# Kernel optimization log

Hardware: AMD Instinct MI355X
Metric: run time of the kernel (lower is better)

Reference implementation:

```python
import jax, jax.numpy as jnp
import numpy as np

# Static multi-scale spatial shapes (H, W) for a 640x640 input, strides [4,8,16,32]
SHAPES = [(160, 160), (80, 80), (40, 40), (20, 20)]
NUM_HEADS, NUM_LEVELS, NUM_POINTS, EMBED_DIM = 8, 4, 4, 256
HEAD_DIM = EMBED_DIM // NUM_HEADS
LEN_V = sum(h * w for h, w in SHAPES)  # 34000


def setup_inputs() -> dict:
    key = jax.random.key(0)
    ks = jax.random.split(key, 12)
    bs, lq = 8, 300
    inp = {
        "query": jax.random.normal(ks[0], (bs, lq, EMBED_DIM), jnp.float32),
        "reference_points": jax.random.uniform(ks[1], (bs, lq, NUM_LEVELS, 2), jnp.float32),
        "value": jax.random.normal(ks[2], (bs, LEN_V, EMBED_DIM), jnp.float32),
        "Wv": jax.random.normal(ks[3], (EMBED_DIM, EMBED_DIM), jnp.float32) * 0.02,
        "bv": jnp.zeros((EMBED_DIM,), jnp.float32),
        "Woff": jax.random.normal(ks[4], (NUM_HEADS * NUM_LEVELS * NUM_POINTS * 2, EMBED_DIM), jnp.float32) * 0.01,
        "boff": jax.random.normal(ks[5], (NUM_HEADS * NUM_LEVELS * NUM_POINTS * 2,), jnp.float32),
        "Wattn": jax.random.normal(ks[6], (NUM_HEADS * NUM_LEVELS * NUM_POINTS, EMBED_DIM), jnp.float32) * 0.02,
        "battn": jnp.zeros((NUM_HEADS * NUM_LEVELS * NUM_POINTS,), jnp.float32),
        "Wout": jax.random.normal(ks[7], (EMBED_DIM, EMBED_DIM), jnp.float32) * 0.02,
        "bout": jnp.zeros((EMBED_DIM,), jnp.float32),
    }
    return inp


def _bilinear_sample(v, loc, H, W):
    """grid_sample(align_corners=False, zero padding) equivalent.
    v:   [bs, H*W, nh, hd] level feature
    loc: [bs, Lq, nh, P, 2] sampling locations in [0, 1]
    returns [bs, Lq, nh, P, hd]
    """
    x = loc[..., 0] * W - 0.5
    y = loc[..., 1] * H - 0.5
    x0 = jnp.floor(x)
    y0 = jnp.floor(y)
    wx = (x - x0)[..., None]
    wy = (y - y0)[..., None]
    x0i = x0.astype(jnp.int32)
    y0i = y0.astype(jnp.int32)

    bs, _, nh, _ = v.shape
    bi = jnp.arange(bs)[:, None, None, None]
    hi = jnp.arange(nh)[None, None, :, None]

    def gather(xi, yi):
        valid = (xi >= 0) & (xi < W) & (yi >= 0) & (yi < H)
        idx = jnp.clip(yi, 0, H - 1) * W + jnp.clip(xi, 0, W - 1)  # [bs,Lq,nh,P]
        g = v[bi, idx, hi]  # [bs,Lq,nh,P,hd]
        return g * valid[..., None].astype(v.dtype)

    g00 = gather(x0i, y0i)
    g01 = gather(x0i + 1, y0i)
    g10 = gather(x0i, y0i + 1)
    g11 = gather(x0i + 1, y0i + 1)
    return (g00 * (1 - wx) * (1 - wy) + g01 * wx * (1 - wy)
            + g10 * (1 - wx) * wy + g11 * wx * wy)


def reference(query, reference_points, value, Wv, bv, Woff, boff, Wattn, battn, Wout, bout):
    bs, lq, _ = query.shape
    nh, nl, npts, hd = NUM_HEADS, NUM_LEVELS, NUM_POINTS, HEAD_DIM

    # value projection -> per-head value
    v = (value @ Wv.T + bv).reshape(bs, -1, nh, hd)

    # sampling offsets and attention weights from the query
    off = (query @ Woff.T + boff).reshape(bs, lq, nh, nl, npts, 2)
    aw = (query @ Wattn.T + battn).reshape(bs, lq, nh, nl * npts)
    aw = jax.nn.softmax(aw, axis=-1).reshape(bs, lq, nh, nl, npts)

    # normalize offsets by (W, H) per level; ref points are 2-d
    normalizer = jnp.array([[w, h] for h, w in SHAPES], jnp.float32)  # [nl,2]
    loc = reference_points[:, :, None, :, None, :] + off / normalizer[None, None, None, :, None, :]

    out = jnp.zeros((bs, lq, nh, hd), query.dtype)
    start = 0
    for l, (H, W) in enumerate(SHAPES):
        v_l = jax.lax.dynamic_slice_in_dim(v, start, H * W, axis=1)
        sampled = _bilinear_sample(v_l, loc[:, :, :, l], H, W)  # [bs,Lq,nh,P,hd]
        out = out + jnp.einsum("bqhp,bqhpd->bqhd", aw[:, :, :, l], sampled)
        start += H * W

    out = out.reshape(bs, lq, nh * hd)
    return out @ Wout.T + bout
```

## Files before the change

kernel.cpp:

```cpp
#include <hip/hip_runtime.h>
#include <hip/hip_bf16.h>


#define BS 8
#define LQ 300
#define LEN_V 34000
#define ED 256
#define NH 8
#define NL 4
#define NP 4

#define VSTRIPS 2125

typedef short short8 __attribute__((ext_vector_type(8)));
typedef short sv4 __attribute__((ext_vector_type(4)));
typedef float f32x4 __attribute__((ext_vector_type(4)));

__device__ __forceinline__ short8 cvt8_reg(float4 a, float4 b) {
  union { short8 v; __hip_bfloat16 h[8]; } u;
  u.h[0] = __float2bfloat16(a.x); u.h[1] = __float2bfloat16(a.y);
  u.h[2] = __float2bfloat16(a.z); u.h[3] = __float2bfloat16(a.w);
  u.h[4] = __float2bfloat16(b.x); u.h[5] = __float2bfloat16(b.y);
  u.h[6] = __float2bfloat16(b.z); u.h[7] = __float2bfloat16(b.w);
  return u.v;
}

__device__ __forceinline__ void cvt8_store(__hip_bfloat16* dst, float4 a, float4 b) {
  *(short8*)dst = cvt8_reg(a, b);
}

__global__ __launch_bounds__(1024, 4) void k_vproj(
    const float* __restrict__ A, const float* __restrict__ B,
    const float* __restrict__ bias, __hip_bfloat16* __restrict__ C) {
  __shared__ __align__(16) __hip_bfloat16 Bs[256][264];
  __shared__ __align__(16) __hip_bfloat16 Cs[32][264];

  const int t = threadIdx.x;

  for (int i = t; i < 256 * 64; i += 1024) {
    const int n = i >> 6;
    const int kf = (i & 63) * 4;
    const float4 b4 = *(const float4*)(B + (size_t)n * ED + kf);
    union { sv4 v; __hip_bfloat16 h[4]; } u;
    u.h[0] = __float2bfloat16(b4.x);
    u.h[1] = __float2bfloat16(b4.y);
    u.h[2] = __float2bfloat16(b4.z);
    u.h[3] = __float2bfloat16(b4.w);
    *(sv4*)&Bs[n][kf] = u.v;
  }
  __syncthreads();

  const int wave = t >> 6;
  const int lane = t & 63;
  const int wr = wave >> 2;
  const int wc = wave & 3;
  const int fr = lane & 15;
  const int fk = (lane >> 4) * 8;
  const int rq = (lane >> 4) * 4;

  float bias_v[4];
#pragma unroll
  for (int ni = 0; ni < 4; ++ni) bias_v[ni] = bias[wc * 64 + ni * 16 + fr];

  for (int strip = blockIdx.x; strip < VSTRIPS; strip += gridDim.x) {
    const size_t row0 = (size_t)strip * 128;
    const float* gA = A + (row0 + wr * 32 + fr) * ED + fk;

    f32x4 acc[2][4];
#pragma unroll
    for (int i = 0; i < 2; ++i)
#pragma unroll
      for (int j = 0; j < 4; ++j) acc[i][j] = (f32x4){0.f, 0.f, 0.f, 0.f};

    float4 c0[2], c1[2];
#pragma unroll
    for (int mi = 0; mi < 2; ++mi) {
      c0[mi] = *(const float4*)(gA + mi * 16 * ED);
      c1[mi] = *(const float4*)(gA + mi * 16 * ED + 4);
    }

    for (int kk = 0; kk < ED; kk += 32) {
      float4 p0[2], p1[2];
      if (kk < ED - 32) {
#pragma unroll
        for (int mi = 0; mi < 2; ++mi) {
          p0[mi] = *(const float4*)(gA + mi * 16 * ED + kk + 32);
          p1[mi] = *(const float4*)(gA + mi * 16 * ED + kk + 36);
        }
      }
      short8 af[2], bf[4];
#pragma unroll
      for (int mi = 0; mi < 2; ++mi) af[mi] = cvt8_reg(c0[mi], c1[mi]);
#pragma unroll
      for (int ni = 0; ni < 4; ++ni)
        bf[ni] = *(const short8*)&Bs[wc * 64 + ni * 16 + fr][kk + fk];
#pragma unroll
      for (int mi = 0; mi < 2; ++mi)
#pragma unroll
        for (int ni = 0; ni < 4; ++ni)
          acc[mi][ni] = __builtin_amdgcn_mfma_f32_16x16x32_bf16(
              af[mi], bf[ni], acc[mi][ni], 0, 0, 0);
#pragma unroll
      for (int mi = 0; mi < 2; ++mi) { c0[mi] = p0[mi]; c1[mi] = p1[mi]; }
    }

#pragma unroll
    for (int p = 0; p < 4; ++p) {
      if (wr == p) {
#pragma unroll
        for (int ni = 0; ni < 4; ++ni) {
          const int col = wc * 64 + ni * 16 + fr;
#pragma unroll
          for (int mi = 0; mi < 2; ++mi) {
            const int rl = mi * 16 + rq;
#pragma unroll
            for (int r = 0; r < 4; ++r)
              Cs[rl + r][col] = __float2bfloat16(acc[mi][ni][r] + bias_v[ni]);
          }
        }
      }
      __syncthreads();
      {
        const int rr = t >> 5;
        const int cb = (t & 31) * 8;
        const size_t gr = row0 + p * 32 + rr;
        *(short8*)(C + gr * ED + cb) = *(const short8*)&Cs[rr][cb];
      }
      __syncthreads();
    }
  }
}

#define LDT64 72

template <typename OutT>
__global__ __launch_bounds__(256) void k_gemm64(
    const float* __restrict__ A, const float* __restrict__ B,
    const float* __restrict__ bias, OutT* __restrict__ C, int M, int ldc) {
  __shared__ __align__(16) __hip_bfloat16 As[64][LDT64];
  __shared__ __align__(16) __hip_bfloat16 Bs[64][LDT64];

  const int t = threadIdx.x;
  const size_t row0 = (size_t)blockIdx.x * 64;
  const int n0 = blockIdx.y * 64;

  const int sr = t >> 2;
  const int sc = (t & 3) * 16;

  const int wave = t >> 6;
  const int lane = t & 63;
  const int mw = (wave & 1) * 32;
  const int nw = (wave >> 1) * 32;
  const int fr = lane & 15;
  const int fk = (lane >> 4) * 8;

  f32x4 acc[2][2];
#pragma unroll
  for (int i = 0; i < 2; ++i)
#pragma unroll
    for (int j = 0; j < 2; ++j) acc[i][j] = (f32x4){0.f, 0.f, 0.f, 0.f};

  const size_t rA = min(row0 + sr, (size_t)(M - 1));
  const float* gA = A + rA * ED + sc;
  const float* gB = B + (size_t)(n0 + sr) * ED + sc;

  for (int kk = 0; kk < ED; kk += 64) {
    float4 a0 = ((const float4*)(gA + kk))[0];
    float4 a1 = ((const float4*)(gA + kk))[1];
    float4 a2 = ((const float4*)(gA + kk))[2];
    float4 a3 = ((const float4*)(gA + kk))[3];
    float4 b0 = ((const float4*)(gB + kk))[0];
    float4 b1 = ((const float4*)(gB + kk))[1];
    float4 b2 = ((const float4*)(gB + kk))[2];
    float4 b3 = ((const float4*)(gB + kk))[3];
    __syncthreads();
    cvt8_store(&As[sr][sc], a0, a1);
    cvt8_store(&As[sr][sc + 8], a2, a3);
    cvt8_store(&Bs[sr][sc], b0, b1);
    cvt8_store(&Bs[sr][sc + 8], b2, b3);
    __syncthreads();

#pragma unroll
    for (int ks = 0; ks < 2; ++ks) {
      short8 afrag[2], bfrag[2];
#pragma unroll
      for (int mi = 0; mi < 2; ++mi)
        afrag[mi] = *(const short8*)&As[mw + mi * 16 + fr][ks * 32 + fk];
#pragma unroll
      for (int ni = 0; ni < 2; ++ni)
        bfrag[ni] = *(const short8*)&Bs[nw + ni * 16 + fr][ks * 32 + fk];
#pragma unroll
      for (int mi = 0; mi < 2; ++mi)
#pragma unroll
        for (int ni = 0; ni < 2; ++ni)
          acc[mi][ni] = __builtin_amdgcn_mfma_f32_16x16x32_bf16(
              afrag[mi], bfrag[ni], acc[mi][ni], 0, 0, 0);
    }
  }

  const int rq = (lane >> 4) * 4;
#pragma unroll
  for (int ni = 0; ni < 2; ++ni) {
    const int col = n0 + nw + ni * 16 + fr;
    const float bias_v = bias[col];
#pragma unroll
    for (int mi = 0; mi < 2; ++mi) {
      const size_t rbase = row0 + mw + mi * 16 + rq;
#pragma unroll
      for (int r = 0; r < 4; ++r) {
        const size_t row = rbase + r;
        if (row < (size_t)M)
          C[row * (size_t)ldc + col] = acc[mi][ni][r] + bias_v;
      }
    }
  }
}

__global__ __launch_bounds__(256) void k_concat(
    const float* __restrict__ Woff, const float* __restrict__ boff,
    const float* __restrict__ Wattn, const float* __restrict__ battn,
    float* __restrict__ Wcat, float* __restrict__ bcat) {
  const int row = blockIdx.x;
  const int t = threadIdx.x;
  const float* src = (row < 256) ? (Woff + (size_t)row * ED)
                                 : (Wattn + (size_t)(row - 256) * ED);
  Wcat[(size_t)row * ED + t] = src[t];
  if (t == 0) bcat[row] = (row < 256) ? boff[row] : battn[row - 256];
}

__global__ __launch_bounds__(256) void k_post(
    const float* __restrict__ refp, float* __restrict__ offs) {
  __shared__ float lg[128];
  const int t = threadIdx.x;
  const int bq = blockIdx.x;
  float* row = offs + (size_t)bq * 384;
  if (t < 128) lg[t] = row[256 + t];
  const float o = row[t];
  const int c = t & 1;
  const int l = (t >> 3) & 3;
  const float norm = (float)(160 >> l);
  const float r = refp[((size_t)bq * NL + l) * 2 + c];
  __syncthreads();
  row[t] = r + o / norm;
  if (t < NH) {
    float m = -1e30f;
#pragma unroll
    for (int i = 0; i < 16; ++i) m = fmaxf(m, lg[t * 16 + i]);
    float e[16];
    float s = 0.f;
#pragma unroll
    for (int i = 0; i < 16; ++i) {
      e[i] = expf(lg[t * 16 + i] - m);
      s += e[i];
    }
    const float inv = 1.f / s;
#pragma unroll
    for (int i = 0; i < 16; ++i) row[256 + t * 16 + i] = e[i] * inv;
  }
}

__device__ __forceinline__ float sample_one(const __hip_bfloat16* __restrict__ vb,
                                            int st, int W, int xi, int yi, int ch) {
  const bool valid = (xi >= 0) & (xi < W) & (yi >= 0) & (yi < W);
  const int xc = min(max(xi, 0), W - 1);
  const int yc = min(max(yi, 0), W - 1);
  const float g = __bfloat162float(vb[((size_t)(st + yc * W + xc)) * ED + ch]);
  return valid ? g : 0.f;
}

__global__ __launch_bounds__(512) void k_sample(
    const __hip_bfloat16* __restrict__ v, const float* __restrict__ offs,
    float* __restrict__ inner) {
  __shared__ float part[16][256];
  __shared__ float slo[256];
  __shared__ float saw[128];
  const int t = threadIdx.x;
  const int bq = blockIdx.x;
  const int b = bq / LQ;
  const float* rowq = offs + (size_t)bq * 384;
  if (t < 256) slo[t] = rowq[t];
  else if (t < 384) saw[t - 256] = rowq[t];
  __syncthreads();

  const int pi = t >> 5;
  const int d = t & 31;
  const int l = pi >> 2;
  const int p = pi & 3;
  const int W = 160 >> l;
  const int st = (l == 0) ? 0 : (l == 1) ? 25600 : (l == 2) ? 32000 : 33600;
  const __hip_bfloat16* vb = v + (size_t)b * LEN_V * ED;

#pragma unroll
  for (int h = 0; h < NH; ++h) {
    const int base = ((h * NL + l) * NP + p) * 2;
    const float lx = slo[base];
    const float ly = slo[base + 1];
    const float w = saw[h * 16 + pi];
    const float x = lx * (float)W - 0.5f;
    const float y = ly * (float)W - 0.5f;
    const float x0f = floorf(x);
    const float y0f = floorf(y);
    const float wx = x - x0f;
    const float wy = y - y0f;
    const int x0 = (int)x0f;
    const int y0 = (int)y0f;
    const int ch = h * 32 + d;
    const float g00 = sample_one(vb, st, W, x0, y0, ch);
    const float g01 = sample_one(vb, st, W, x0 + 1, y0, ch);
    const float g10 = sample_one(vb, st, W, x0, y0 + 1, ch);
    const float g11 = sample_one(vb, st, W, x0 + 1, y0 + 1, ch);
    const float vxy = (g00 * (1.f - wx) + g01 * wx) * (1.f - wy) +
                      (g10 * (1.f - wx) + g11 * wx) * wy;
    part[pi][ch] = w * vxy;
  }
  __syncthreads();
  if (t < 256) {
    float s = 0.f;
#pragma unroll
    for (int q = 0; q < 16; ++q) s += part[q][t];
    inner[(size_t)bq * ED + t] = s;
  }
}

extern "C" void kernel_launch(void* const* d_in, const int* in_sizes, int n_in,
                              void* d_out, int out_size, void* d_ws, size_t ws_size,
                              hipStream_t stream) {
  const float* query = (const float*)d_in[0];
  const float* refp  = (const float*)d_in[1];
  const float* value = (const float*)d_in[2];
  const float* Wv    = (const float*)d_in[3];
  const float* bv    = (const float*)d_in[4];
  const float* Woff  = (const float*)d_in[5];
  const float* boff  = (const float*)d_in[6];
  const float* Wattn = (const float*)d_in[7];
  const float* battn = (const float*)d_in[8];
  const float* Wout  = (const float*)d_in[9];
  const float* bout  = (const float*)d_in[10];
  float* out = (float*)d_out;

  char* ws = (char*)d_ws;
  __hip_bfloat16* v = (__hip_bfloat16*)ws;
  size_t off = (size_t)BS * LEN_V * ED * 2;
  float* offs = (float*)(ws + off);
  off += (size_t)BS * LQ * 384 * 4;
  float* inner = (float*)(ws + off);
  off += (size_t)BS * LQ * 256 * 4;
  float* Wcat = (float*)(ws + off);
  off += (size_t)384 * ED * 4;
  float* bcat = (float*)(ws + off);

  const int M_Q = BS * LQ;

  k_concat<<<384, 256, 0, stream>>>(Woff, boff, Wattn, battn, Wcat, bcat);
  k_vproj<<<256, 1024, 0, stream>>>(value, Wv, bv, v);
  k_gemm64<float><<<dim3(38, 6), 256, 0, stream>>>(
      query, Wcat, bcat, offs, M_Q, 384);
  k_post<<<M_Q, 256, 0, stream>>>(refp, offs);
  k_sample<<<M_Q, 512, 0, stream>>>(v, offs, inner);
  k_gemm64<float><<<dim3(38, 4), 256, 0, stream>>>(
      inner, Wout, bout, out, M_Q, ED);
}
```

Baseline: 507.7 us.

## Deepen A-prefetch across strips and store vproj output directly from registers

Reworks the value-projection kernel's main loop into a fully unrolled 8-step K loop with a two-stage register double buffer. The loads for the next strip are issued during the last steps of the current one, so global latency is hidden across strip boundaries. Swapping the MFMA operands makes each lane hold four consecutive output columns, so results plus bias are written straight to global memory as 8-byte stores. This removes the shared-memory staging buffer and its per-strip __syncthreads calls. The cost is more live registers and narrower global stores than the previous 16-byte coalesced writes.

```diff
diff --git a/kernel.cpp b/kernel.cpp
--- a/kernel.cpp
+++ b/kernel.cpp
@@ -33,7 +33,6 @@
     const float* __restrict__ A, const float* __restrict__ B,
     const float* __restrict__ bias, __hip_bfloat16* __restrict__ C) {
   __shared__ __align__(16) __hip_bfloat16 Bs[256][264];
-  __shared__ __align__(16) __hip_bfloat16 Cs[32][264];
 
   const int t = threadIdx.x;
 
@@ -56,15 +55,33 @@
   const int wc = wave & 3;
   const int fr = lane & 15;
   const int fk = (lane >> 4) * 8;
-  const int rq = (lane >> 4) * 4;
-
-  float bias_v[4];
-#pragma unroll
-  for (int ni = 0; ni < 4; ++ni) bias_v[ni] = bias[wc * 64 + ni * 16 + fr];
-
-  for (int strip = blockIdx.x; strip < VSTRIPS; strip += gridDim.x) {
-    const size_t row0 = (size_t)strip * 128;
-    const float* gA = A + (row0 + wr * 32 + fr) * ED + fk;
+  const int nq = (lane >> 4) * 4;
+
+  float4 bias_v[4];
+#pragma unroll
+  for (int ni = 0; ni < 4; ++ni)
+    bias_v[ni] = *(const float4*)(bias + wc * 64 + ni * 16 + nq);
+
+  int strip = blockIdx.x;
+  if (strip >= VSTRIPS) return;
+
+  size_t row0 = (size_t)strip * 128;
+  const float* gA = A + (row0 + wr * 32 + fr) * ED + fk;
+
+  float4 c0[2][2], c1[2][2];
+#pragma unroll
+  for (int s = 0; s < 2; ++s)
+#pragma unroll
+    for (int mi = 0; mi < 2; ++mi) {
+      c0[s][mi] = *(const float4*)(gA + mi * 16 * ED + s * 32);
+      c1[s][mi] = *(const float4*)(gA + mi * 16 * ED + s * 32 + 4);
+    }
+
+  while (true) {
+    const int next = strip + (int)gridDim.x;
+    const bool have_next = next < VSTRIPS;
+    const size_t nrow0 = (size_t)(have_next ? next : strip) * 128;
+    const float* gAn = A + (nrow0 + wr * 32 + fr) * ED + fk;
 
     f32x4 acc[2][4];
 #pragma unroll
@@ -72,25 +89,20 @@
 #pragma unroll
       for (int j = 0; j < 4; ++j) acc[i][j] = (f32x4){0.f, 0.f, 0.f, 0.f};
 
-    float4 c0[2], c1[2];
-#pragma unroll
-    for (int mi = 0; mi < 2; ++mi) {
-      c0[mi] = *(const float4*)(gA + mi * 16 * ED);
-      c1[mi] = *(const float4*)(gA + mi * 16 * ED + 4);
-    }
-
-    for (int kk = 0; kk < ED; kk += 32) {
-      float4 p0[2], p1[2];
-      if (kk < ED - 32) {
-#pragma unroll
-        for (int mi = 0; mi < 2; ++mi) {
-          p0[mi] = *(const float4*)(gA + mi * 16 * ED + kk + 32);
-          p1[mi] = *(const float4*)(gA + mi * 16 * ED + kk + 36);
-        }
+#pragma unroll
+    for (int s = 0; s < 8; ++s) {
+      const int b = s & 1;
+      const int kk = s * 32;
+      short8 af[2];
+#pragma unroll
+      for (int mi = 0; mi < 2; ++mi) af[mi] = cvt8_reg(c0[b][mi], c1[b][mi]);
+      const float* src = (s < 6) ? (gA + kk + 64) : (gAn + (s - 6) * 32);
+#pragma unroll
+      for (int mi = 0; mi < 2; ++mi) {
+        c0[b][mi] = *(const float4*)(src + mi * 16 * ED);
+        c1[b][mi] = *(const float4*)(src + mi * 16 * ED + 4);
       }
-      short8 af[2], bf[4];
-#pragma unroll
-      for (int mi = 0; mi < 2; ++mi) af[mi] = cvt8_reg(c0[mi], c1[mi]);
+      short8 bf[4];
 #pragma unroll
       for (int ni = 0; ni < 4; ++ni)
         bf[ni] = *(const short8*)&Bs[wc * 64 + ni * 16 + fr][kk + fk];
@@ -99,35 +111,28 @@
 #pragma unroll
         for (int ni = 0; ni < 4; ++ni)
           acc[mi][ni] = __builtin_amdgcn_mfma_f32_16x16x32_bf16(
-              af[mi], bf[ni], acc[mi][ni], 0, 0, 0);
-#pragma unroll
-      for (int mi = 0; mi < 2; ++mi) { c0[mi] = p0[mi]; c1[mi] = p1[mi]; }
-    }
-
-#pragma unroll
-    for (int p = 0; p < 4; ++p) {
-      if (wr == p) {
-#pragma unroll
-        for (int ni = 0; ni < 4; ++ni) {
-          const int col = wc * 64 + ni * 16 + fr;
-#pragma unroll
-          for (int mi = 0; mi < 2; ++mi) {
-            const int rl = mi * 16 + rq;
-#pragma unroll
-            for (int r = 0; r < 4; ++r)
-              Cs[rl + r][col] = __float2bfloat16(acc[mi][ni][r] + bias_v[ni]);
-          }
-        }
+              bf[ni], af[mi], acc[mi][ni], 0, 0, 0);
+    }
+
+#pragma unroll
+    for (int mi = 0; mi < 2; ++mi) {
+      __hip_bfloat16* crow =
+          C + (row0 + wr * 32 + mi * 16 + fr) * (size_t)ED + wc * 64 + nq;
+#pragma unroll
+      for (int ni = 0; ni < 4; ++ni) {
+        union { sv4 v; __hip_bfloat16 h[4]; } u;
+        u.h[0] = __float2bfloat16(acc[mi][ni][0] + bias_v[ni].x);
+        u.h[1] = __float2bfloat16(acc[mi][ni][1] + bias_v[ni].y);
+        u.h[2] = __float2bfloat16(acc[mi][ni][2] + bias_v[ni].z);
+        u.h[3] = __float2bfloat16(acc[mi][ni][3] + bias_v[ni].w);
+        *(sv4*)(crow + ni * 16) = u.v;
       }
-      __syncthreads();
-      {
-        const int rr = t >> 5;
-        const int cb = (t & 31) * 8;
-        const size_t gr = row0 + p * 32 + rr;
-        *(short8*)(C + gr * ED + cb) = *(const short8*)&Cs[rr][cb];
-      }
-      __syncthreads();
-    }
+    }
+
+    if (!have_next) break;
+    strip = next;
+    row0 = nrow0;
+    gA = gAn;
   }
 }
 
```

New measurement: 670.8 us. +32.1%, slower.

## Convert Wv to bf16 once and run vproj as one 64-row tile per block

Applied to the files above, without the earlier changes.

The value projection kernel no longer stages the full bf16 weight matrix in LDS or loops persistently over 128-row strips. Wv is converted to bf16 once in the concat kernel, and each of 4250 blocks of 512 threads computes a 64-row tile, reading B fragments straight from global memory (served by L2) and writing through a single LDS staging pass. This removes the per-block weight conversion and the repeated barriers, and raises occupancy. The cost is more global and L2 traffic for the weight fragments and the overhead of launching many more blocks.

```diff
diff --git a/kernel.cpp b/kernel.cpp
--- a/kernel.cpp
+++ b/kernel.cpp
@@ -10,8 +10,6 @@
 #define NL 4
 #define NP 4
 
-#define VSTRIPS 2125
-
 typedef short short8 __attribute__((ext_vector_type(8)));
 typedef short sv4 __attribute__((ext_vector_type(4)));
 typedef float f32x4 __attribute__((ext_vector_type(4)));
@@ -29,27 +27,12 @@
   *(short8*)dst = cvt8_reg(a, b);
 }
 
-__global__ __launch_bounds__(1024, 4) void k_vproj(
-    const float* __restrict__ A, const float* __restrict__ B,
+__global__ __launch_bounds__(512, 8) void k_vproj(
+    const float* __restrict__ A, const __hip_bfloat16* __restrict__ Wb,
     const float* __restrict__ bias, __hip_bfloat16* __restrict__ C) {
-  __shared__ __align__(16) __hip_bfloat16 Bs[256][264];
-  __shared__ __align__(16) __hip_bfloat16 Cs[32][264];
-
-  const int t = threadIdx.x;
-
-  for (int i = t; i < 256 * 64; i += 1024) {
-    const int n = i >> 6;
-    const int kf = (i & 63) * 4;
-    const float4 b4 = *(const float4*)(B + (size_t)n * ED + kf);
-    union { sv4 v; __hip_bfloat16 h[4]; } u;
-    u.h[0] = __float2bfloat16(b4.x);
-    u.h[1] = __float2bfloat16(b4.y);
-    u.h[2] = __float2bfloat16(b4.z);
-    u.h[3] = __float2bfloat16(b4.w);
-    *(sv4*)&Bs[n][kf] = u.v;
-  }
-  __syncthreads();
-
+  __shared__ __align__(16) __hip_bfloat16 Cs[64][264];
+
+  const int t = threadIdx.x;
   const int wave = t >> 6;
   const int lane = t & 63;
   const int wr = wave >> 2;
@@ -58,76 +41,72 @@
   const int fk = (lane >> 4) * 8;
   const int rq = (lane >> 4) * 4;
 
+  const size_t row0 = (size_t)blockIdx.x * 64;
+  const float* gA = A + (row0 + wr * 32 + fr) * ED + fk;
+  const __hip_bfloat16* gB = Wb + (size_t)(wc * 64 + fr) * ED + fk;
+
   float bias_v[4];
 #pragma unroll
   for (int ni = 0; ni < 4; ++ni) bias_v[ni] = bias[wc * 64 + ni * 16 + fr];
 
-  for (int strip = blockIdx.x; strip < VSTRIPS; strip += gridDim.x) {
-    const size_t row0 = (size_t)strip * 128;
-    const float* gA = A + (row0 + wr * 32 + fr) * ED + fk;
-
-    f32x4 acc[2][4];
-#pragma unroll
-    for (int i = 0; i < 2; ++i)
-#pragma unroll
-      for (int j = 0; j < 4; ++j) acc[i][j] = (f32x4){0.f, 0.f, 0.f, 0.f};
-
-    float4 c0[2], c1[2];
-#pragma unroll
-    for (int mi = 0; mi < 2; ++mi) {
-      c0[mi] = *(const float4*)(gA + mi * 16 * ED);
-      c1[mi] = *(const float4*)(gA + mi * 16 * ED + 4);
-    }
-
-    for (int kk = 0; kk < ED; kk += 32) {
-      float4 p0[2], p1[2];
-      if (kk < ED - 32) {
-#pragma unroll
-        for (int mi = 0; mi < 2; ++mi) {
-          p0[mi] = *(const float4*)(gA + mi * 16 * ED + kk + 32);
-          p1[mi] = *(const float4*)(gA + mi * 16 * ED + kk + 36);
-        }
+  f32x4 acc[2][4];
+#pragma unroll
+  for (int i = 0; i < 2; ++i)
+#pragma unroll
+    for (int j = 0; j < 4; ++j) acc[i][j] = (f32x4){0.f, 0.f, 0.f, 0.f};
+
+  float4 c0[2], c1[2];
+#pragma unroll
+  for (int mi = 0; mi < 2; ++mi) {
+    c0[mi] = *(const float4*)(gA + mi * 16 * ED);
+    c1[mi] = *(const float4*)(gA + mi * 16 * ED + 4);
+  }
+
+#pragma unroll
+  for (int s = 0; s < 8; ++s) {
+    const int kk = s * 32;
+    float4 p0[2], p1[2];
+    if (s < 7) {
+#pragma unroll
+      for (int mi = 0; mi < 2; ++mi) {
+        p0[mi] = *(const float4*)(gA + mi * 16 * ED + kk + 32);
+        p1[mi] = *(const float4*)(gA + mi * 16 * ED + kk + 36);
       }
-      short8 af[2], bf[4];
-#pragma unroll
-      for (int mi = 0; mi < 2; ++mi) af[mi] = cvt8_reg(c0[mi], c1[mi]);
+    }
+    short8 af[2], bf[4];
+#pragma unroll
+    for (int mi = 0; mi < 2; ++mi) af[mi] = cvt8_reg(c0[mi], c1[mi]);
+#pragma unroll
+    for (int ni = 0; ni < 4; ++ni)
+      bf[ni] = *(const short8*)(gB + (size_t)ni * 16 * ED + kk);
+#pragma unroll
+    for (int mi = 0; mi < 2; ++mi)
 #pragma unroll
       for (int ni = 0; ni < 4; ++ni)
-        bf[ni] = *(const short8*)&Bs[wc * 64 + ni * 16 + fr][kk + fk];
-#pragma unroll
-      for (int mi = 0; mi < 2; ++mi)
-#pragma unroll
-        for (int ni = 0; ni < 4; ++ni)
-          acc[mi][ni] = __builtin_amdgcn_mfma_f32_16x16x32_bf16(
-              af[mi], bf[ni], acc[mi][ni], 0, 0, 0);
+        acc[mi][ni] = __builtin_amdgcn_mfma_f32_16x16x32_bf16(
+            af[mi], bf[ni], acc[mi][ni], 0, 0, 0);
+    if (s < 7) {
 #pragma unroll
       for (int mi = 0; mi < 2; ++mi) { c0[mi] = p0[mi]; c1[mi] = p1[mi]; }
     }
-
-#pragma unroll
-    for (int p = 0; p < 4; ++p) {
-      if (wr == p) {
-#pragma unroll
-        for (int ni = 0; ni < 4; ++ni) {
-          const int col = wc * 64 + ni * 16 + fr;
-#pragma unroll
-          for (int mi = 0; mi < 2; ++mi) {
-            const int rl = mi * 16 + rq;
-#pragma unroll
-            for (int r = 0; r < 4; ++r)
-              Cs[rl + r][col] = __float2bfloat16(acc[mi][ni][r] + bias_v[ni]);
-          }
-        }
-      }
-      __syncthreads();
-      {
-        const int rr = t >> 5;
-        const int cb = (t & 31) * 8;
-        const size_t gr = row0 + p * 32 + rr;
-        *(short8*)(C + gr * ED + cb) = *(const short8*)&Cs[rr][cb];
-      }
-      __syncthreads();
-    }
+  }
+
+#pragma unroll
+  for (int mi = 0; mi < 2; ++mi)
+#pragma unroll
+    for (int ni = 0; ni < 4; ++ni) {
+      const int col = wc * 64 + ni * 16 + fr;
+      const int rb = wr * 32 + mi * 16 + rq;
+#pragma unroll
+      for (int r = 0; r < 4; ++r)
+        Cs[rb + r][col] = __float2bfloat16(acc[mi][ni][r] + bias_v[ni]);
+    }
+  __syncthreads();
+#pragma unroll
+  for (int p = 0; p < 4; ++p) {
+    const int rr = p * 16 + (t >> 5);
+    const int cb = (t & 31) * 8;
+    *(short8*)(C + (row0 + rr) * ED + cb) = *(const short8*)&Cs[rr][cb];
   }
 }
 
@@ -219,13 +198,19 @@
 __global__ __launch_bounds__(256) void k_concat(
     const float* __restrict__ Woff, const float* __restrict__ boff,
     const float* __restrict__ Wattn, const float* __restrict__ battn,
-    float* __restrict__ Wcat, float* __restrict__ bcat) {
+    float* __restrict__ Wcat, float* __restrict__ bcat,
+    const float* __restrict__ Wv, __hip_bfloat16* __restrict__ Wb) {
   const int row = blockIdx.x;
   const int t = threadIdx.x;
-  const float* src = (row < 256) ? (Woff + (size_t)row * ED)
-                                 : (Wattn + (size_t)(row - 256) * ED);
-  Wcat[(size_t)row * ED + t] = src[t];
-  if (t == 0) bcat[row] = (row < 256) ? boff[row] : battn[row - 256];
+  if (row < 384) {
+    const float* src = (row < 256) ? (Woff + (size_t)row * ED)
+                                   : (Wattn + (size_t)(row - 256) * ED);
+    Wcat[(size_t)row * ED + t] = src[t];
+    if (t == 0) bcat[row] = (row < 256) ? boff[row] : battn[row - 256];
+  } else {
+    const int n = row - 384;
+    Wb[(size_t)n * ED + t] = __float2bfloat16(Wv[(size_t)n * ED + t]);
+  }
 }
 
 __global__ __launch_bounds__(256) void k_post(
@@ -348,11 +333,13 @@
   float* Wcat = (float*)(ws + off);
   off += (size_t)384 * ED * 4;
   float* bcat = (float*)(ws + off);
+  off += 2048;
+  __hip_bfloat16* Wb = (__hip_bfloat16*)(ws + off);
 
   const int M_Q = BS * LQ;
 
-  k_concat<<<384, 256, 0, stream>>>(Woff, boff, Wattn, battn, Wcat, bcat);
-  k_vproj<<<256, 1024, 0, stream>>>(value, Wv, bv, v);
+  k_concat<<<640, 256, 0, stream>>>(Woff, boff, Wattn, battn, Wcat, bcat, Wv, Wb);
+  k_vproj<<<4250, 512, 0, stream>>>(value, Wb, bv, v);
   k_gemm64<float><<<dim3(38, 6), 256, 0, stream>>>(
       query, Wcat, bcat, offs, M_Q, 384);
   k_post<<<M_Q, 256, 0, stream>>>(refp, offs);
```

New measurement: 859.2 us. 69.2% more time.
